# Optimization experiments

Measured on AMD Instinct MI355X. Metric: run time of the kernel, lower is better.

The kernel has to match this reference:

```python
import jax, jax.numpy as jnp
from jax import lax
import numpy as np
import math

V, D, N, L, KC, KL, B, S = 32000, 1024, 64, 4, 4, 4, 2, 1024
SCALE = 1.0 / math.sqrt(2 * L)   # base_layer.residual_scale
GAMMA = 0.01                     # lindblad_gamma
COND_TH = 100.0                  # condition_threshold
PHASE = np.complex64(np.exp(1j * 0.1))  # quaternionic escape rotation


def setup_inputs() -> dict:
    key = jax.random.key(0)
    ks = jax.random.split(key, 16)
    g = lambda k, shp, s=0.02: jax.random.normal(k, shp, jnp.float32) * s
    return {
        'token_ids': jax.random.randint(ks[0], (B, S), 0, V, dtype=jnp.int32),
        'emb_r': g(ks[1], (V, D)),
        'emb_i': g(ks[2], (V, D)),
        'W_in': g(ks[3], (L, D, 2 * D)),
        'conv_k': g(ks[4], (L, D, KC), 0.2),
        'A_log': jax.random.normal(ks[5], (L, D, N), jnp.float32) * 0.5,
        'dt_scale': g(ks[6], (L, D), 1.0),
        'dt_bias': jnp.full((L, D), -2.0, jnp.float32),
        'W_B': g(ks[7], (L, N, D)),
        'W_C': g(ks[8], (L, N, D)),
        'D_skip': g(ks[9], (L, D), 0.1),
        'W_out': g(ks[10], (L, D, D)),
        'L_ops': g(ks[11], (L, KL, D), 0.1),
        'norm_w': jnp.ones((D,), jnp.float32),
    }


def _dwconv(x, k):
    # causal depthwise conv; x [B,S,D] real, k [D,KC]
    xt = jnp.transpose(x, (0, 2, 1))  # [B,D,S]
    pad = k.shape[-1] - 1
    y = lax.conv_general_dilated(xt, k[:, None, :], (1,), [(pad, 0)],
                                 feature_group_count=k.shape[0])
    return jnp.transpose(y, (0, 2, 1))


def _csilu(x):
    # complex 'silu': x * sigmoid(|x|)
    return x * jax.nn.sigmoid(jnp.abs(x))


def _layer(x, Wi, ck, Alog, dts, dtb, WB, WC, Dk, Wo, Lops):
    residual = x
    xz = jnp.einsum('bsd,de->bse', x, Wi)          # complex [B,S,2D]
    x1, z = xz[..., :D], xz[..., D:]
    x1 = _dwconv(x1.real, ck) + 1j * _dwconv(x1.imag, ck)
    x1 = _csilu(x1)
    dt = jax.nn.softplus(x1.real * dts + dtb)      # [B,S,D] real
    A = -jnp.exp(Alog)                             # [D,N] real, stable
    Bc = jnp.einsum('bsd,nd->bsn', x1, WB)         # complex [B,S,N]
    Cc = jnp.einsum('bsd,nd->bsn', x1, WC)

    def step(h, inp):
        dt_t, x_t, B_t, C_t = inp                  # [B,D],[B,D],[B,N],[B,N]
        decay = jnp.exp(dt_t[..., None] * A)       # [B,D,N] real
        h = decay * h + (dt_t * x_t)[..., None] * B_t[:, None, :]
        y = jnp.einsum('bdn,bn->bd', h, C_t)
        return h, y

    h0 = jnp.zeros((x.shape[0], D, N), jnp.complex64)
    xs = (jnp.transpose(dt, (1, 0, 2)), jnp.transpose(x1, (1, 0, 2)),
          jnp.transpose(Bc, (1, 0, 2)), jnp.transpose(Cc, (1, 0, 2)))
    _, ys = lax.scan(step, h0, xs)                 # [S,B,D]
    y = jnp.transpose(ys, (1, 0, 2)) + Dk * x1
    y = y * _csilu(z)
    branch = jnp.einsum('bsd,de->bse', y, Wo)      # branch_out = (out-res)/scale

    # Lindblad dissipation: psi -> psi - gamma * sum_k L_k (L_k^H psi)
    proj = jnp.einsum('bsd,kd->bsk', branch, Lops)
    branch = branch - GAMMA * jnp.einsum('bsk,kd->bsd', proj, Lops)

    # H_eff = mean_s |psi_s><psi_s|; quaternionic escape uses its conditioning.
    # Only the diagonal is needed for the (diag-approx) condition number.
    diag = jnp.mean(jnp.abs(branch) ** 2, axis=1)  # [B,D]
    cond = jnp.max(diag, -1) / (jnp.min(diag, -1) + 1e-8)
    phase = jnp.where(cond > COND_TH, PHASE, jnp.complex64(1.0))  # [B]
    branch = branch * phase[:, None, None]

    # hybrid automata: _H_prev is None on first forward -> no jump (faithful)
    return residual + SCALE * branch


def reference(token_ids, emb_r, emb_i, W_in, conv_k, A_log, dt_scale, dt_bias,
              W_B, W_C, D_skip, W_out, L_ops, norm_w):
    psi = emb_r[token_ids] + 1j * emb_i[token_ids]   # [B,S,D] complex64
    for l in range(L):
        psi = _layer(psi, W_in[l], conv_k[l], A_log[l], dt_scale[l],
                     dt_bias[l], W_B[l], W_C[l], D_skip[l], W_out[l], L_ops[l])
    # ComplexRMSNorm
    rms = jnp.sqrt(jnp.mean(jnp.abs(psi) ** 2, -1, keepdims=True) + 1e-8)
    psi = psi / rms * norm_w
    # Born collapse sampler with weight tied to real embedding
    amp_r = jnp.einsum('bsd,vd->bsv', psi.real, emb_r)
    amp_i = jnp.einsum('bsd,vd->bsv', psi.imag, emb_r)
    logits = jnp.log(amp_r ** 2 + amp_i ** 2 + 1e-8)  # [B,S,V] real
    return logits
```

## Files before the change

kernel.cpp:

```cpp
#include <hip/hip_runtime.h>
#include <math.h>

#define BB 2
#define SS 1024
#define DD 1024
#define NN 64
#define LLAYERS 4
#define KCC 4
#define KLL 4
#define VV 32000
#define MM (BB*SS)
#define M2 (2*MM)
#define PS ((size_t)MM*DD)
#define CH 4
#define LC (SS/CH)
#define BDW (BB*DD)

#define SCALE_F 0.35355339059327373f
#define GAMMA_F 0.01f
#define PHASE_COS 0.99500416527802576f
#define PHASE_SIN 0.09983341664682815f

typedef _Float16 f16x8 __attribute__((ext_vector_type(8)));
typedef _Float16 f16x4 __attribute__((ext_vector_type(4)));
typedef float f32x4 __attribute__((ext_vector_type(4)));

__device__ __forceinline__ float softplus_f(float x) {
    return fmaxf(x, 0.f) + log1pf(expf(-fabsf(x)));
}

__device__ __forceinline__ void async16(void* lds_dst, const void* g_src) {
    __builtin_amdgcn_global_load_lds(
        (const __attribute__((address_space(1))) unsigned int*)g_src,
        (__attribute__((address_space(3))) unsigned int*)lds_dst,
        16, 0, 0);
}

__device__ __forceinline__ float rsum64_dpp(float v) {
    int x;
    x = __float_as_int(v);
    v += __int_as_float(__builtin_amdgcn_update_dpp(0, x, 0x111, 0xf, 0xf, true));
    x = __float_as_int(v);
    v += __int_as_float(__builtin_amdgcn_update_dpp(0, x, 0x112, 0xf, 0xf, true));
    x = __float_as_int(v);
    v += __int_as_float(__builtin_amdgcn_update_dpp(0, x, 0x114, 0xf, 0xf, true));
    x = __float_as_int(v);
    v += __int_as_float(__builtin_amdgcn_update_dpp(0, x, 0x118, 0xf, 0xf, true));
    x = __float_as_int(v);
    v += __int_as_float(__builtin_amdgcn_update_dpp(0, x, 0x142, 0xa, 0xf, true));
    x = __float_as_int(v);
    v += __int_as_float(__builtin_amdgcn_update_dpp(0, x, 0x143, 0xc, 0xf, true));
    return v;
}

__global__ __launch_bounds__(256) void k_split_w(const float* __restrict__ W,
        _Float16* __restrict__ Wh, _Float16* __restrict__ Wl, int Ksz, int Nsz) {
    __shared__ float t[32][33];
    int k0 = blockIdx.x * 32, n0 = blockIdx.y * 32;
    size_t base = (size_t)blockIdx.z * Ksz * Nsz;
    int r = threadIdx.x >> 3, c4 = (threadIdx.x & 7) * 4;
    float4 v = *(const float4*)(W + base + (size_t)(k0 + r) * Nsz + n0 + c4);
    t[r][c4 + 0] = v.x; t[r][c4 + 1] = v.y; t[r][c4 + 2] = v.z; t[r][c4 + 3] = v.w;
    __syncthreads();
    f16x4 hi, lo;
    #pragma unroll
    for (int j = 0; j < 4; ++j) {
        float x = t[c4 + j][r];
        _Float16 h = (_Float16)x;
        hi[j] = h; lo[j] = (_Float16)(x - (float)h);
    }
    size_t o = base + (size_t)(n0 + r) * Ksz + k0 + c4;
    *(f16x4*)(Wh + o) = hi;
    *(f16x4*)(Wl + o) = lo;
}

__global__ __launch_bounds__(256) void k_embed(const int* __restrict__ tok,
        const float* __restrict__ er, const float* __restrict__ ei,
        float* __restrict__ Pr, float* __restrict__ Pi,
        _Float16* __restrict__ Ph, _Float16* __restrict__ Pl) {
    int i = blockIdx.x * 256 + threadIdx.x;
    int d4 = (i & (DD/4 - 1)) * 4;
    int m  = i >> 8;
    int t = tok[m];
    float4 r  = *(const float4*)(er + (size_t)t * DD + d4);
    float4 im = *(const float4*)(ei + (size_t)t * DD + d4);
    size_t o = (size_t)m * DD + d4;
    *(float4*)(Pr + o) = r;
    *(float4*)(Pi + o) = im;
    float vr[4] = {r.x, r.y, r.z, r.w}, vi[4] = {im.x, im.y, im.z, im.w};
    f16x4 rh, rl, ih, il;
    #pragma unroll
    for (int j = 0; j < 4; ++j) {
        _Float16 h = (_Float16)vr[j]; rh[j] = h; rl[j] = (_Float16)(vr[j] - (float)h);
        _Float16 g = (_Float16)vi[j]; ih[j] = g; il[j] = (_Float16)(vi[j] - (float)g);
    }
    *(f16x4*)(Ph + o) = rh;      *(f16x4*)(Pl + o) = rl;
    *(f16x4*)(Ph + PS + o) = ih; *(f16x4*)(Pl + PS + o) = il;
}

__global__ __launch_bounds__(256, 2) void k_gemm_f16(
        const _Float16* __restrict__ Ah, const _Float16* __restrict__ Al,
        const _Float16* __restrict__ Bh, const _Float16* __restrict__ Bl,
        float* __restrict__ C, int Nsz) {
    __shared__ __align__(16) unsigned char lds[32768];
    const int lane = threadIdx.x & 63;
    const int wid  = threadIdx.x >> 6;
    const int wm = (wid >> 1) * 64;
    const int wv = (wid & 1) * 64;
    const int n0 = blockIdx.x * 128;
    const int m0 = blockIdx.y * 128;
    const int fr = lane & 15, fq = lane >> 4;

    f32x4 acc[4][4] = {};

    for (int k0 = 0; k0 < 1024; k0 += 32) {
        #pragma unroll
        for (int j = 0; j < 8; ++j) {
            int cid = wid * 8 + j;
            int sel = cid >> 3, c = cid & 7;
            const _Float16* bp = (sel == 0) ? Ah : (sel == 1) ? Al : (sel == 2) ? Bh : Bl;
            int rbase = ((sel < 2) ? m0 : n0) + c * 16 + fr;
            async16(lds + cid * 1024, bp + (size_t)rbase * 1024 + k0 + fq * 8);
        }
        __syncthreads();

        f16x8 ah[4], al[4];
        #pragma unroll
        for (int ms = 0; ms < 4; ++ms) {
            int off = ((wm >> 4) + ms) * 1024 + lane * 16;
            ah[ms] = *(const f16x8*)(lds + off);
            al[ms] = *(const f16x8*)(lds + 8192 + off);
        }
        #pragma unroll
        for (int vs = 0; vs < 4; ++vs) {
            int boff = ((wv >> 4) + vs) * 1024 + lane * 16;
            f16x8 bh = *(const f16x8*)(lds + 16384 + boff);
            f16x8 bl = *(const f16x8*)(lds + 24576 + boff);
            #pragma unroll
            for (int ms = 0; ms < 4; ++ms) {
                acc[ms][vs] = __builtin_amdgcn_mfma_f32_16x16x32_f16(ah[ms], bh, acc[ms][vs], 0, 0, 0);
                acc[ms][vs] = __builtin_amdgcn_mfma_f32_16x16x32_f16(ah[ms], bl, acc[ms][vs], 0, 0, 0);
                acc[ms][vs] = __builtin_amdgcn_mfma_f32_16x16x32_f16(al[ms], bh, acc[ms][vs], 0, 0, 0);
            }
        }
        __syncthreads();
    }

    #pragma unroll
    for (int ms = 0; ms < 4; ++ms) {
        #pragma unroll
        for (int vs = 0; vs < 4; ++vs) {
            #pragma unroll
            for (int r = 0; r < 4; ++r) {
                int row = m0 + wm + ms * 16 + fq * 4 + r;
                int col = n0 + wv + vs * 16 + fr;
                C[(size_t)row * Nsz + col] = acc[ms][vs][r];
            }
        }
    }
}

__global__ __launch_bounds__(256, 2) void k_gemm_n64(
        const _Float16* __restrict__ Ah, const _Float16* __restrict__ Al,
        const _Float16* __restrict__ Bh, const _Float16* __restrict__ Bl,
        float* __restrict__ C, int Nsz) {
    __shared__ __align__(16) unsigned char lds[24576];
    const int lane = threadIdx.x & 63;
    const int wid  = threadIdx.x >> 6;
    const int wm = (wid >> 1) * 64;
    const int wv = (wid & 1) * 32;
    const int n0 = blockIdx.x * 64;
    const int m0 = blockIdx.y * 128;
    const int fr = lane & 15, fq = lane >> 4;

    f32x4 acc[4][2] = {};

    for (int k0 = 0; k0 < 1024; k0 += 32) {
        #pragma unroll
        for (int j = 0; j < 6; ++j) {
            int cid = j * 4 + wid;
            const _Float16* bp;
            int rbase, ldsoff;
            if (cid < 16) {
                bp = (cid >> 3) ? Al : Ah;
                rbase = m0 + (cid & 7) * 16 + fr;
                ldsoff = cid * 1024;
            } else {
                int r = cid - 16;
                bp = (r >> 2) ? Bl : Bh;
                rbase = n0 + (r & 3) * 16 + fr;
                ldsoff = 16384 + r * 1024;
            }
            async16(lds + ldsoff, bp + (size_t)rbase * 1024 + k0 + fq * 8);
        }
        __syncthreads();

        f16x8 ah[4], al[4];
        #pragma unroll
        for (int ms = 0; ms < 4; ++ms) {
            int off = ((wm >> 4) + ms) * 1024 + lane * 16;
            ah[ms] = *(const f16x8*)(lds + off);
            al[ms] = *(const f16x8*)(lds + 8192 + off);
        }
        #pragma unroll
        for (int vs = 0; vs < 2; ++vs) {
            int boff = ((wv >> 4) + vs) * 1024 + lane * 16;
            f16x8 bh = *(const f16x8*)(lds + 16384 + boff);
            f16x8 bl = *(const f16x8*)(lds + 20480 + boff);
            #pragma unroll
            for (int ms = 0; ms < 4; ++ms) {
                acc[ms][vs] = __builtin_amdgcn_mfma_f32_16x16x32_f16(ah[ms], bh, acc[ms][vs], 0, 0, 0);
                acc[ms][vs] = __builtin_amdgcn_mfma_f32_16x16x32_f16(ah[ms], bl, acc[ms][vs], 0, 0, 0);
                acc[ms][vs] = __builtin_amdgcn_mfma_f32_16x16x32_f16(al[ms], bh, acc[ms][vs], 0, 0, 0);
            }
        }
        __syncthreads();
    }

    #pragma unroll
    for (int ms = 0; ms < 4; ++ms) {
        #pragma unroll
        for (int vs = 0; vs < 2; ++vs) {
            #pragma unroll
            for (int r = 0; r < 4; ++r) {
                int row = m0 + wm + ms * 16 + fq * 4 + r;
                int col = n0 + wv + vs * 16 + fr;
                C[(size_t)row * Nsz + col] = acc[ms][vs][r];
            }
        }
    }
}

__global__ __launch_bounds__(256) void k_conv(const float* __restrict__ XZ,
        const float* __restrict__ ck, const float* __restrict__ dts,
        const float* __restrict__ dtb,
        float* __restrict__ Xr, float* __restrict__ Xi, float* __restrict__ DT,
        float* __restrict__ ZUr, float* __restrict__ ZUi) {
    int i4 = blockIdx.x * 256 + threadIdx.x;
    int dq = (i4 & (DD / 4 - 1)) * 4;
    int m  = i4 >> 8;
    int b = m >> 10, s = m & (SS - 1);
    size_t i = (size_t)m * DD + dq;
    float kw[4][4];
    #pragma unroll
    for (int c = 0; c < 4; ++c)
        *(float4*)kw[c] = *(const float4*)(ck + (size_t)(dq + c) * KCC);
    float cr[4] = {0.f, 0.f, 0.f, 0.f}, ci[4] = {0.f, 0.f, 0.f, 0.f};
    #pragma unroll
    for (int j = 0; j < KCC; ++j) {
        int sj = s - (KCC - 1) + j;
        if (sj >= 0) {
            size_t mm = ((size_t)(b << 10) + sj) * 2048 + dq;
            float4 xr4 = *(const float4*)(XZ + mm);
            float4 xi4 = *(const float4*)(XZ + (size_t)MM * 2048 + mm);
            float xr_[4] = {xr4.x, xr4.y, xr4.z, xr4.w};
            float xi_[4] = {xi4.x, xi4.y, xi4.z, xi4.w};
            #pragma unroll
            for (int c = 0; c < 4; ++c) {
                cr[c] = fmaf(xr_[c], kw[c][j], cr[c]);
                ci[c] = fmaf(xi_[c], kw[c][j], ci[c]);
            }
        }
    }
    float4 dts4 = *(const float4*)(dts + dq);
    float4 dtb4 = *(const float4*)(dtb + dq);
    float dts_[4] = {dts4.x, dts4.y, dts4.z, dts4.w};
    float dtb_[4] = {dtb4.x, dtb4.y, dtb4.z, dtb4.w};
    float xro[4], xio[4], dto[4];
    #pragma unroll
    for (int c = 0; c < 4; ++c) {
        float mag = sqrtf(cr[c] * cr[c] + ci[c] * ci[c]);
        float sg = 1.f / (1.f + expf(-mag));
        xro[c] = cr[c] * sg; xio[c] = ci[c] * sg;
        dto[c] = softplus_f(fmaf(xro[c], dts_[c], dtb_[c]));
    }
    *(float4*)(Xr + i) = make_float4(xro[0], xro[1], xro[2], xro[3]);
    *(float4*)(Xi + i) = make_float4(xio[0], xio[1], xio[2], xio[3]);
    *(float4*)(DT + i) = make_float4(dto[0], dto[1], dto[2], dto[3]);
    float4 zr4 = *(const float4*)(XZ + (size_t)m * 2048 + DD + dq);
    float4 zi4 = *(const float4*)(XZ + (size_t)(MM + m) * 2048 + DD + dq);
    float zr_[4] = {zr4.x, zr4.y, zr4.z, zr4.w};
    float zi_[4] = {zi4.x, zi4.y, zi4.z, zi4.w};
    float zur[4], zui[4];
    #pragma unroll
    for (int c = 0; c < 4; ++c) {
        float mz = sqrtf(zr_[c] * zr_[c] + zi_[c] * zi_[c]);
        float sz = 1.f / (1.f + expf(-mz));
        zur[c] = zr_[c] * sz; zui[c] = zi_[c] * sz;
    }
    *(float4*)(ZUr + i) = make_float4(zur[0], zur[1], zur[2], zur[3]);
    *(float4*)(ZUi + i) = make_float4(zui[0], zui[1], zui[2], zui[3]);
}

__global__ __launch_bounds__(256) void k_bc(const float* __restrict__ X,
        const float* __restrict__ WBp, const float* __restrict__ WCp,
        float* __restrict__ BC2) {
    __shared__ float xs[4][DD];
    __shared__ float red[4 * 256];
    int r0 = blockIdx.x * 4;
    for (int f = threadIdx.x; f < 4 * (DD / 4); f += 256) {
        int r = f / (DD / 4), c = (f % (DD / 4)) * 4;
        *(float4*)(&xs[r][c]) = *(const float4*)(X + (size_t)(r0 + r) * DD + c);
    }
    __syncthreads();
    int out = threadIdx.x & 127;
    int half = threadIdx.x >> 7;
    const float* Wrow = (out < 64) ? (WBp + (size_t)out * DD) : (WCp + (size_t)(out - 64) * DD);
    float acc[4] = {0.f, 0.f, 0.f, 0.f};
    for (int k = half * 512; k < half * 512 + 512; k += 4) {
        float4 w = *(const float4*)(Wrow + k);
        #pragma unroll
        for (int r = 0; r < 4; ++r) {
            float4 x4 = *(float4*)(&xs[r][k]);
            acc[r] = fmaf(x4.x, w.x, fmaf(x4.y, w.y, fmaf(x4.z, w.z, fmaf(x4.w, w.w, acc[r]))));
        }
    }
    #pragma unroll
    for (int r = 0; r < 4; ++r) red[r * 256 + threadIdx.x] = acc[r];
    __syncthreads();
    if (threadIdx.x < 128) {
        int isIm = (r0 >= MM) ? 1 : 0;
        int n = out & 63;
        int comp = ((out >> 6) << 1) | isIm;
        #pragma unroll
        for (int r = 0; r < 4; ++r) {
            float v = red[r * 256 + threadIdx.x] + red[r * 256 + threadIdx.x + 128];
            int m = (r0 + r) & (MM - 1);
            BC2[((size_t)m * 64 + n) * 4 + comp] = v;
        }
    }
}

__global__ __launch_bounds__(256, 8) void k_scan1(const float* __restrict__ X,
        const float* __restrict__ DT, const float4* __restrict__ BC2,
        const float* __restrict__ Alog, float* __restrict__ Y2T,
        float2* __restrict__ HB, float* __restrict__ SDT) {
    int w = (blockIdx.x << 2) + (threadIdx.x >> 6);
    int lane = threadIdx.x & 63;
    int c = w & (CH - 1);
    int bd = w >> 2;
    int b = bd >> 10, d = bd & (DD - 1);
    float Av = -__expf(Alog[(size_t)d * NN + lane]);
    float hr = 0.f, hi = 0.f, sdt = 0.f;
    int s0 = c * LC, s1 = s0 + LC;
    size_t mBase = (size_t)(b << 10);
    size_t md = (mBase + s0) * DD + d;
    float dt_c = DT[md], xr_c = X[md], xi_c = X[PS + md];
    float4 bc_c = BC2[(mBase + s0) * 64 + lane];
    size_t ys = (size_t)bd * SS + s0;
    for (int s = s0; s < s1; ++s) {
        int sn = (s + 1 < s1) ? (s + 1) : s;
        size_t mdn = (mBase + sn) * DD + d;
        float dt_n = DT[mdn], xr_n = X[mdn], xi_n = X[PS + mdn];
        float4 bc_n = BC2[(mBase + sn) * 64 + lane];
        float g = __expf(dt_c * Av);
        float dxr = dt_c * xr_c, dxi = dt_c * xi_c;
        hr = fmaf(g, hr, fmaf(dxr, bc_c.x, -dxi * bc_c.y));
        hi = fmaf(g, hi, fmaf(dxr, bc_c.y,  dxi * bc_c.x));
        sdt += dt_c;
        float yr = rsum64_dpp(hr * bc_c.z - hi * bc_c.w);
        float yi = rsum64_dpp(hr * bc_c.w + hi * bc_c.z);
        if (lane == 63) {
            Y2T[ys]      = yr;
            Y2T[PS + ys] = yi;
        }
        ++ys;
        dt_c = dt_n; xr_c = xr_n; xi_c = xi_n; bc_c = bc_n;
    }
    HB[((size_t)c * BDW + bd) * NN + lane] = make_float2(hr, hi);
    if (lane == 0) SDT[c * BDW + bd] = sdt;
}

__global__ __launch_bounds__(256, 8) void k_scan3(const float* __restrict__ DT,
        const float* __restrict__ BC2, const float* __restrict__ Alog,
        const float2* __restrict__ HB, const float* __restrict__ SDT,
        float* __restrict__ Y2T) {
    int w = (blockIdx.x << 2) + (threadIdx.x >> 6);
    int lane = threadIdx.x & 63;
    int cm1 = w >> 11;
    int bd = w & (BDW - 1);
    int b = bd >> 10, d = bd & (DD - 1);
    float Av = -__expf(Alog[(size_t)d * NN + lane]);
    float2 h0 = HB[(size_t)bd * NN + lane];
    float hr = h0.x, hi = h0.y;
    if (cm1 >= 1) {
        float2 h1 = HB[((size_t)1 * BDW + bd) * NN + lane];
        float P1 = __expf(Av * SDT[1 * BDW + bd]);
        hr = fmaf(P1, hr, h1.x); hi = fmaf(P1, hi, h1.y);
        if (cm1 >= 2) {
            float2 h2 = HB[((size_t)2 * BDW + bd) * NN + lane];
            float P2 = __expf(Av * SDT[2 * BDW + bd]);
            hr = fmaf(P2, hr, h2.x); hi = fmaf(P2, hi, h2.y);
        }
    }
    int s0 = (cm1 + 1) * LC, s1 = s0 + LC;
    size_t mBase = (size_t)(b << 10);
    size_t md = (mBase + s0) * DD + d;
    float dt_c = DT[md];
    float2 cc_c = *(const float2*)(BC2 + ((mBase + s0) * 64 + lane) * 4 + 2);
    size_t ys = (size_t)bd * SS + s0;
    for (int s = s0; s < s1; ++s) {
        int sn = (s + 1 < s1) ? (s + 1) : s;
        size_t mdn = (mBase + sn) * DD + d;
        float dt_n = DT[mdn];
        float2 cc_n = *(const float2*)(BC2 + ((mBase + sn) * 64 + lane) * 4 + 2);
        float g = __expf(dt_c * Av);
        hr *= g; hi *= g;
        float yr = rsum64_dpp(hr * cc_c.x - hi * cc_c.y);
        float yi = rsum64_dpp(hr * cc_c.y + hi * cc_c.x);
        if (lane == 63) {
            Y2T[ys]      += yr;
            Y2T[PS + ys] += yi;
        }
        ++ys;
        dt_c = dt_n; cc_c = cc_n;
    }
}

__global__ __launch_bounds__(256) void k_ymod(const float* __restrict__ Y2T,
        const float* __restrict__ X, const float* __restrict__ ZUr,
        const float* __restrict__ ZUi, const float* __restrict__ Dk,
        _Float16* __restrict__ YOh, _Float16* __restrict__ YOl) {
    __shared__ float tr[64][65];
    __shared__ float ti[64][65];
    int d0 = blockIdx.x * 64, m0 = blockIdx.y * 64;
    int b = m0 >> 10, s0 = m0 & (SS - 1);
    int t = threadIdx.x;
    int rr = t >> 2, c0 = (t & 3) * 4;
    size_t ybase = (size_t)(b * DD + d0 + rr) * SS + s0;
    #pragma unroll
    for (int j = 0; j < 4; ++j) {
        float4 vr = *(const float4*)(Y2T + ybase + c0 + j * 16);
        float4 vi = *(const float4*)(Y2T + PS + ybase + c0 + j * 16);
        int sl = c0 + j * 16;
        tr[sl + 0][rr] = vr.x; tr[sl + 1][rr] = vr.y; tr[sl + 2][rr] = vr.z; tr[sl + 3][rr] = vr.w;
        ti[sl + 0][rr] = vi.x; ti[sl + 1][rr] = vi.y; ti[sl + 2][rr] = vi.z; ti[sl + 3][rr] = vi.w;
    }
    __syncthreads();
    int td = t & 63, tq = t >> 6;
    float dk = Dk[d0 + td];
    #pragma unroll
    for (int k = 0; k < 16; ++k) {
        int tm = tq * 16 + k;
        size_t i = (size_t)(m0 + tm) * DD + d0 + td;
        float yr = tr[tm][td];
        float yi = ti[tm][td];
        yr = fmaf(dk, X[i], yr);
        yi = fmaf(dk, X[PS + i], yi);
        float zr = ZUr[i], zi = ZUi[i];
        float or_ = yr * zr - yi * zi;
        float oi_ = yr * zi + yi * zr;
        _Float16 h0 = (_Float16)or_, h1 = (_Float16)oi_;
        YOh[i] = h0;      YOl[i] = (_Float16)(or_ - (float)h0);
        YOh[PS + i] = h1; YOl[PS + i] = (_Float16)(oi_ - (float)h1);
    }
}

__global__ __launch_bounds__(256) void k_projcorr(float* __restrict__ BR,
        const float* __restrict__ Lop) {
    int row = (blockIdx.x << 2) + (threadIdx.x >> 6);
    int lane = threadIdx.x & 63;
    float* br = BR + (size_t)row * DD;
    float4 v[4], lw[4][4];
    float acc[4] = {0.f, 0.f, 0.f, 0.f};
    #pragma unroll
    for (int j = 0; j < 4; ++j) {
        int col = lane * 4 + j * 256;
        v[j] = *(const float4*)(br + col);
        #pragma unroll
        for (int k = 0; k < 4; ++k) {
            lw[j][k] = *(const float4*)(Lop + (size_t)k * DD + col);
            acc[k] += v[j].x * lw[j][k].x + v[j].y * lw[j][k].y
                    + v[j].z * lw[j][k].z + v[j].w * lw[j][k].w;
        }
    }
    #pragma unroll
    for (int off = 1; off <= 32; off <<= 1) {
        #pragma unroll
        for (int k = 0; k < 4; ++k) acc[k] += __shfl_xor(acc[k], off, 64);
    }
    #pragma unroll
    for (int j = 0; j < 4; ++j) {
        int col = lane * 4 + j * 256;
        float4 o;
        o.x = v[j].x - GAMMA_F * (acc[0]*lw[j][0].x + acc[1]*lw[j][1].x + acc[2]*lw[j][2].x + acc[3]*lw[j][3].x);
        o.y = v[j].y - GAMMA_F * (acc[0]*lw[j][0].y + acc[1]*lw[j][1].y + acc[2]*lw[j][2].y + acc[3]*lw[j][3].y);
        o.z = v[j].z - GAMMA_F * (acc[0]*lw[j][0].z + acc[1]*lw[j][1].z + acc[2]*lw[j][2].z + acc[3]*lw[j][3].z);
        o.w = v[j].w - GAMMA_F * (acc[0]*lw[j][0].w + acc[1]*lw[j][1].w + acc[2]*lw[j][2].w + acc[3]*lw[j][3].w);
        *(float4*)(br + col) = o;
    }
}

__global__ __launch_bounds__(256) void k_diag(const float* __restrict__ BR,
        float* __restrict__ DG) {
    __shared__ float red[4][64];
    int b = blockIdx.y, d0 = blockIdx.x * 64;
    int sg = threadIdx.x >> 6, ld = threadIdx.x & 63;
    float acc = 0.f;
    for (int s = sg; s < SS; s += 4) {
        size_t m = (size_t)(b * SS + s) * DD + d0 + ld;
        float r = BR[m], ii = BR[PS + m];
        acc = fmaf(r, r, fmaf(ii, ii, acc));
    }
    red[sg][ld] = acc;
    __syncthreads();
    if (threadIdx.x < 64) {
        float v = red[0][threadIdx.x] + red[1][threadIdx.x] + red[2][threadIdx.x] + red[3][threadIdx.x];
        DG[b * DD + d0 + threadIdx.x] = v * (1.f / SS);
    }
}

__global__ __launch_bounds__(256) void k_phase(const float* __restrict__ DG,
        float* __restrict__ PH) {
    __shared__ float mx[256], mn[256];
    int b = blockIdx.x;
    float vmax = -1e30f, vmin = 1e30f;
    for (int d = threadIdx.x; d < DD; d += 256) {
        float v = DG[b * DD + d];
        vmax = fmaxf(vmax, v); vmin = fminf(vmin, v);
    }
    mx[threadIdx.x] = vmax; mn[threadIdx.x] = vmin;
    __syncthreads();
    for (int st = 128; st >= 1; st >>= 1) {
        if (threadIdx.x < st) {
            mx[threadIdx.x] = fmaxf(mx[threadIdx.x], mx[threadIdx.x + st]);
            mn[threadIdx.x] = fminf(mn[threadIdx.x], mn[threadIdx.x + st]);
        }
        __syncthreads();
    }
    if (threadIdx.x == 0) {
        float cond = mx[0] / (mn[0] + 1e-8f);
        bool ap = cond > 100.0f;
        PH[b * 2 + 0] = ap ? PHASE_COS : 1.f;
        PH[b * 2 + 1] = ap ? PHASE_SIN : 0.f;
    }
}

__global__ __launch_bounds__(256) void k_resid(float* __restrict__ Pr,
        float* __restrict__ Pi, const float* __restrict__ BR,
        const float* __restrict__ PH,
        _Float16* __restrict__ Ph, _Float16* __restrict__ Pl) {
    size_t i = ((size_t)blockIdx.x * 256 + threadIdx.x) * 4;
    int b = (int)(i >> 20);
    float pr = PH[b * 2], pih = PH[b * 2 + 1];
    float4 brr4 = *(const float4*)(BR + i);
    float4 bri4 = *(const float4*)(BR + PS + i);
    float4 pr4  = *(const float4*)(Pr + i);
    float4 pi4  = *(const float4*)(Pi + i);
    float brr[4] = {brr4.x, brr4.y, brr4.z, brr4.w};
    float bri[4] = {bri4.x, bri4.y, bri4.z, bri4.w};
    float pro[4] = {pr4.x, pr4.y, pr4.z, pr4.w};
    float pio[4] = {pi4.x, pi4.y, pi4.z, pi4.w};
    f16x4 rh, rl, ih, il;
    float nr[4], ni[4];
    #pragma unroll
    for (int c = 0; c < 4; ++c) {
        nr[c] = fmaf(SCALE_F, brr[c] * pr - bri[c] * pih, pro[c]);
        ni[c] = fmaf(SCALE_F, brr[c] * pih + bri[c] * pr, pio[c]);
        _Float16 h0 = (_Float16)nr[c]; rh[c] = h0; rl[c] = (_Float16)(nr[c] - (float)h0);
        _Float16 h1 = (_Float16)ni[c]; ih[c] = h1; il[c] = (_Float16)(ni[c] - (float)h1);
    }
    *(float4*)(Pr + i) = make_float4(nr[0], nr[1], nr[2], nr[3]);
    *(float4*)(Pi + i) = make_float4(ni[0], ni[1], ni[2], ni[3]);
    *(f16x4*)(Ph + i) = rh;      *(f16x4*)(Pl + i) = rl;
    *(f16x4*)(Ph + PS + i) = ih; *(f16x4*)(Pl + PS + i) = il;
}

__global__ __launch_bounds__(256) void k_rms(const float* __restrict__ Pr,
        const float* __restrict__ Pi, const float* __restrict__ nw,
        _Float16* __restrict__ Sp) {
    __shared__ float red[256];
    int m = blockIdx.x;
    int d = threadIdx.x * 4;
    float4 r  = *(const float4*)(Pr + (size_t)m * DD + d);
    float4 ii = *(const float4*)(Pi + (size_t)m * DD + d);
    float acc = r.x*r.x + r.y*r.y + r.z*r.z + r.w*r.w
              + ii.x*ii.x + ii.y*ii.y + ii.z*ii.z + ii.w*ii.w;
    red[threadIdx.x] = acc;
    __syncthreads();
    for (int st = 128; st >= 1; st >>= 1) {
        if (threadIdx.x < st) red[threadIdx.x] += red[threadIdx.x + st];
        __syncthreads();
    }
    float inv = 1.f / sqrtf(red[0] * (1.f / DD) + 1e-8f);
    float4 w = *(const float4*)(nw + d);
    float qr[4] = {r.x*inv*w.x, r.y*inv*w.y, r.z*inv*w.z, r.w*inv*w.w};
    float qi[4] = {ii.x*inv*w.x, ii.y*inv*w.y, ii.z*inv*w.z, ii.w*inv*w.w};
    f16x4 rh, rl, ih, il;
    #pragma unroll
    for (int j = 0; j < 4; ++j) {
        _Float16 h = (_Float16)qr[j]; rh[j] = h; rl[j] = (_Float16)(qr[j] - (float)h);
        _Float16 g = (_Float16)qi[j]; ih[j] = g; il[j] = (_Float16)(qi[j] - (float)g);
    }
    size_t o = (size_t)m * DD + d;
    *(f16x4*)(Sp + o)          = rh;
    *(f16x4*)(Sp + PS + o)     = rl;
    *(f16x4*)(Sp + 2 * PS + o) = ih;
    *(f16x4*)(Sp + 3 * PS + o) = il;
}

__global__ __launch_bounds__(256) void k_split_e(const float* __restrict__ E,
        _Float16* __restrict__ Eh, _Float16* __restrict__ El) {
    size_t i = (size_t)(blockIdx.x * 256 + threadIdx.x) * 8;
    float4 a = *(const float4*)(E + i);
    float4 b = *(const float4*)(E + i + 4);
    float v[8] = {a.x, a.y, a.z, a.w, b.x, b.y, b.z, b.w};
    f16x8 hi, lo;
    #pragma unroll
    for (int j = 0; j < 8; ++j) {
        _Float16 h = (_Float16)v[j];
        hi[j] = h; lo[j] = (_Float16)(v[j] - (float)h);
    }
    *(f16x8*)(Eh + i) = hi;
    *(f16x8*)(El + i) = lo;
}

__global__ __launch_bounds__(256, 2) void k_logits_mfma(
        const _Float16* __restrict__ Sp,
        const _Float16* __restrict__ Eh, const _Float16* __restrict__ El,
        float* __restrict__ out) {
    __shared__ __align__(16) unsigned char lds[49152];
    const int lane = threadIdx.x & 63;
    const int wid  = threadIdx.x >> 6;
    const int wm = (wid >> 1) * 64;
    const int wv = (wid & 1) * 64;
    const int fr = lane & 15, fq = lane >> 4;
    int x = blockIdx.x & 7;
    int j = blockIdx.x >> 3;
    const int m0 = ((x << 1) | (j & 1)) << 7;
    const int v0 = (j >> 1) << 7;

    f32x4 accR[4][4] = {};
    f32x4 accI[4][4] = {};

    for (int k0 = 0; k0 < DD; k0 += 32) {
        #pragma unroll
        for (int jj = 0; jj < 12; ++jj) {
            int cid = jj * 4 + wid;
            const _Float16* src;
            int ldsoff;
            if (cid < 32) {
                int p = cid >> 3, c = cid & 7;
                src = Sp + (size_t)p * PS + (size_t)(m0 + c * 16 + fr) * DD + k0 + fq * 8;
                ldsoff = p * 8192 + c * 1024;
            } else {
                int r = cid - 32;
                int q = r >> 3, c = r & 7;
                const _Float16* Ep = q ? El : Eh;
                src = Ep + (size_t)(v0 + c * 16 + fr) * DD + k0 + fq * 8;
                ldsoff = 32768 + q * 8192 + c * 1024;
            }
            async16(lds + ldsoff, src);
        }
        __syncthreads();

        f16x8 aRh[4], aRl[4], aIh[4], aIl[4];
        #pragma unroll
        for (int ms = 0; ms < 4; ++ms) {
            int off = ((wm >> 4) + ms) * 1024 + lane * 16;
            aRh[ms] = *(const f16x8*)(lds + off);
            aRl[ms] = *(const f16x8*)(lds + 8192 + off);
            aIh[ms] = *(const f16x8*)(lds + 16384 + off);
            aIl[ms] = *(const f16x8*)(lds + 24576 + off);
        }
        #pragma unroll
        for (int vs = 0; vs < 4; ++vs) {
            int boff = ((wv >> 4) + vs) * 1024 + lane * 16;
            f16x8 bh = *(const f16x8*)(lds + 32768 + boff);
            f16x8 bl = *(const f16x8*)(lds + 40960 + boff);
            #pragma unroll
            for (int ms = 0; ms < 4; ++ms) {
                accR[ms][vs] = __builtin_amdgcn_mfma_f32_16x16x32_f16(aRh[ms], bh, accR[ms][vs], 0, 0, 0);
                accR[ms][vs] = __builtin_amdgcn_mfma_f32_16x16x32_f16(aRh[ms], bl, accR[ms][vs], 0, 0, 0);
                accR[ms][vs] = __builtin_amdgcn_mfma_f32_16x16x32_f16(aRl[ms], bh, accR[ms][vs], 0, 0, 0);
                accI[ms][vs] = __builtin_amdgcn_mfma_f32_16x16x32_f16(aIh[ms], bh, accI[ms][vs], 0, 0, 0);
                accI[ms][vs] = __builtin_amdgcn_mfma_f32_16x16x32_f16(aIh[ms], bl, accI[ms][vs], 0, 0, 0);
                accI[ms][vs] = __builtin_amdgcn_mfma_f32_16x16x32_f16(aIl[ms], bh, accI[ms][vs], 0, 0, 0);
            }
        }
        __syncthreads();
    }

    #pragma unroll
    for (int ms = 0; ms < 4; ++ms) {
        #pragma unroll
        for (int vs = 0; vs < 4; ++vs) {
            #pragma unroll
            for (int r = 0; r < 4; ++r) {
                int row = m0 + wm + ms * 16 + fq * 4 + r;
                int col = v0 + wv + vs * 16 + fr;
                float ar = accR[ms][vs][r], ai = accI[ms][vs][r];
                __builtin_nontemporal_store(logf(fmaf(ar, ar, fmaf(ai, ai, 1e-8f))),
                                            out + (size_t)row * VV + col);
            }
        }
    }
}

extern "C" void kernel_launch(void* const* d_in, const int* in_sizes, int n_in,
                              void* d_out, int out_size, void* d_ws, size_t ws_size,
                              hipStream_t stream) {
    const int*   tok  = (const int*)d_in[0];
    const float* er   = (const float*)d_in[1];
    const float* ei   = (const float*)d_in[2];
    const float* Win  = (const float*)d_in[3];
    const float* ck   = (const float*)d_in[4];
    const float* Alog = (const float*)d_in[5];
    const float* dts  = (const float*)d_in[6];
    const float* dtb  = (const float*)d_in[7];
    const float* WB   = (const float*)d_in[8];
    const float* WC   = (const float*)d_in[9];
    const float* Dk   = (const float*)d_in[10];
    const float* Wo   = (const float*)d_in[11];
    const float* Lop  = (const float*)d_in[12];
    const float* nw   = (const float*)d_in[13];
    float* out = (float*)d_out;

    float* W0   = (float*)d_ws;
    float* P    = W0;
    float* XZ   = W0 + 2 * PS;
    float* X    = W0 + 6 * PS;
    float* DTp  = W0 + 8 * PS;
    float* ZU   = W0 + 9 * PS;
    float* Y2T  = W0 + 11 * PS;
    _Float16* YOh = (_Float16*)(W0 + 19 * PS);
    _Float16* YOl = (_Float16*)(W0 + 20 * PS);
    _Float16* Ph  = (_Float16*)(W0 + 21 * PS);
    _Float16* Pl  = (_Float16*)(W0 + 22 * PS);
    float* BR   = XZ;
    float* BC2  = W0 + 23 * PS;
    float* DIAG = BC2 + (size_t)MM * 64 * 4;
    float* PH   = DIAG + BB * DD;
    float2* HB  = (float2*)(PH + 16);
    float* SDT  = (float*)(HB + (size_t)CH * BDW * NN);
    _Float16* Winh = (_Float16*)(W0 + 25 * PS);
    _Float16* Winl = (_Float16*)(W0 + 27 * PS);
    _Float16* Woh  = (_Float16*)(W0 + 29 * PS);
    _Float16* Wol  = (_Float16*)(W0 + 30 * PS);
    _Float16* Sp  = (_Float16*)(W0 + 2 * PS);
    _Float16* Ehp = (_Float16*)(W0 + 4 * PS);
    _Float16* Elp = (_Float16*)(W0 + 13 * PS);

    k_split_w<<<dim3(32, 64, 4), 256, 0, stream>>>(Win, Winh, Winl, 1024, 2048);
    k_split_w<<<dim3(32, 32, 4), 256, 0, stream>>>(Wo, Woh, Wol, 1024, 1024);

    k_embed<<<(int)(PS / 4 / 256), 256, 0, stream>>>(tok, er, ei, P, P + PS, Ph, Pl);

    for (int l = 0; l < LLAYERS; ++l) {
        const float* Lopl = Lop + (size_t)l * KLL * DD;
        const float* Alogl = Alog + (size_t)l * DD * NN;
        const _Float16* Wih = Winh + (size_t)l * 2048 * 1024;
        const _Float16* Wil = Winl + (size_t)l * 2048 * 1024;
        const _Float16* Wohl = Woh + (size_t)l * 1024 * 1024;
        const _Float16* Woll = Wol + (size_t)l * 1024 * 1024;

        k_gemm_f16<<<dim3(2048 / 128, M2 / 128), 256, 0, stream>>>(Ph, Pl, Wih, Wil, XZ, 2048);
        k_conv<<<(int)(MM * (size_t)DD / 4 / 256), 256, 0, stream>>>(XZ, ck + (size_t)l * DD * KCC,
                dts + l * DD, dtb + l * DD, X, X + PS, DTp, ZU, ZU + PS);
        k_bc<<<M2 / 4, 256, 0, stream>>>(X, WB + (size_t)l * NN * DD, WC + (size_t)l * NN * DD, BC2);
        k_scan1<<<(BDW * CH) / 4, 256, 0, stream>>>(X, DTp, (const float4*)BC2, Alogl, Y2T, HB, SDT);
        k_scan3<<<(BDW * 3) / 4, 256, 0, stream>>>(DTp, BC2, Alogl, HB, SDT, Y2T);
        k_ymod<<<dim3(DD / 64, MM / 64), 256, 0, stream>>>(Y2T, X, ZU, ZU + PS, Dk + l * DD, YOh, YOl);
        k_gemm_n64<<<dim3(1024 / 64, M2 / 128), 256, 0, stream>>>(YOh, YOl, Wohl, Woll, BR, 1024);
        k_projcorr<<<M2 / 4, 256, 0, stream>>>(BR, Lopl);
        k_diag<<<dim3(DD / 64, BB), 256, 0, stream>>>(BR, DIAG);
        k_phase<<<BB, 256, 0, stream>>>(DIAG, PH);
        k_resid<<<(int)(PS / 4 / 256), 256, 0, stream>>>(P, P + PS, BR, PH, Ph, Pl);
    }

    k_rms<<<MM, 256, 0, stream>>>(P, P + PS, nw, Sp);
    k_split_e<<<(int)((size_t)VV * DD / 8 / 256), 256, 0, stream>>>(er, Ehp, Elp);
    k_logits_mfma<<<4000, 256, 0, stream>>>(Sp, Ehp, Elp, out);
}
```

Baseline: 3.594 ms.

## Process four channels per wavefront in chunked scan to reuse B/C loads

The chunked selective-scan kernels now give each wavefront four adjacent D channels instead of one. Each per-timestep B/C vector load is shared across the four channels, and dt/x are read as float4. This cuts redundant global traffic on BC2 and the per-step load latency per channel, at the cost of 4x fewer wavefronts and more registers, which may hurt latency hiding. The logits store also drops its nontemporal hint and becomes a plain store, and a parameter is renamed to avoid a clash with the new macro.

```diff
diff --git a/kernel.cpp b/kernel.cpp
--- a/kernel.cpp
+++ b/kernel.cpp
@@ -15,6 +15,7 @@
 #define CH 4
 #define LC (SS/CH)
 #define BDW (BB*DD)
+#define DG 4
 
 #define SCALE_F 0.35355339059327373f
 #define GAMMA_F 0.01f
@@ -331,86 +332,115 @@
     }
 }
 
-__global__ __launch_bounds__(256, 8) void k_scan1(const float* __restrict__ X,
+__global__ __launch_bounds__(256) void k_scan1(const float* __restrict__ X,
         const float* __restrict__ DT, const float4* __restrict__ BC2,
         const float* __restrict__ Alog, float* __restrict__ Y2T,
         float2* __restrict__ HB, float* __restrict__ SDT) {
     int w = (blockIdx.x << 2) + (threadIdx.x >> 6);
     int lane = threadIdx.x & 63;
     int c = w & (CH - 1);
-    int bd = w >> 2;
-    int b = bd >> 10, d = bd & (DD - 1);
-    float Av = -__expf(Alog[(size_t)d * NN + lane]);
-    float hr = 0.f, hi = 0.f, sdt = 0.f;
+    int grp = w >> 2;
+    int b = grp >> 8;
+    int d0 = (grp & 255) << 2;
+    float Av[DG], hr[DG], hi[DG], sdt[DG];
+    #pragma unroll
+    for (int j = 0; j < DG; ++j) {
+        Av[j] = -__expf(Alog[(size_t)(d0 + j) * NN + lane]);
+        hr[j] = 0.f; hi[j] = 0.f; sdt[j] = 0.f;
+    }
     int s0 = c * LC, s1 = s0 + LC;
     size_t mBase = (size_t)(b << 10);
-    size_t md = (mBase + s0) * DD + d;
-    float dt_c = DT[md], xr_c = X[md], xi_c = X[PS + md];
+    size_t md = (mBase + s0) * DD + d0;
+    float4 dt_c = *(const float4*)(DT + md);
+    float4 xr_c = *(const float4*)(X + md);
+    float4 xi_c = *(const float4*)(X + PS + md);
     float4 bc_c = BC2[(mBase + s0) * 64 + lane];
-    size_t ys = (size_t)bd * SS + s0;
+    size_t ys = ((size_t)(b << 10) + d0) * SS + s0;
     for (int s = s0; s < s1; ++s) {
         int sn = (s + 1 < s1) ? (s + 1) : s;
-        size_t mdn = (mBase + sn) * DD + d;
-        float dt_n = DT[mdn], xr_n = X[mdn], xi_n = X[PS + mdn];
+        size_t mdn = (mBase + sn) * DD + d0;
+        float4 dt_n = *(const float4*)(DT + mdn);
+        float4 xr_n = *(const float4*)(X + mdn);
+        float4 xi_n = *(const float4*)(X + PS + mdn);
         float4 bc_n = BC2[(mBase + sn) * 64 + lane];
-        float g = __expf(dt_c * Av);
-        float dxr = dt_c * xr_c, dxi = dt_c * xi_c;
-        hr = fmaf(g, hr, fmaf(dxr, bc_c.x, -dxi * bc_c.y));
-        hi = fmaf(g, hi, fmaf(dxr, bc_c.y,  dxi * bc_c.x));
-        sdt += dt_c;
-        float yr = rsum64_dpp(hr * bc_c.z - hi * bc_c.w);
-        float yi = rsum64_dpp(hr * bc_c.w + hi * bc_c.z);
-        if (lane == 63) {
-            Y2T[ys]      = yr;
-            Y2T[PS + ys] = yi;
+        float dtv[4] = {dt_c.x, dt_c.y, dt_c.z, dt_c.w};
+        float xrv[4] = {xr_c.x, xr_c.y, xr_c.z, xr_c.w};
+        float xiv[4] = {xi_c.x, xi_c.y, xi_c.z, xi_c.w};
+        #pragma unroll
+        for (int j = 0; j < DG; ++j) {
+            float g = __expf(dtv[j] * Av[j]);
+            float dxr = dtv[j] * xrv[j], dxi = dtv[j] * xiv[j];
+            hr[j] = fmaf(g, hr[j], fmaf(dxr, bc_c.x, -dxi * bc_c.y));
+            hi[j] = fmaf(g, hi[j], fmaf(dxr, bc_c.y,  dxi * bc_c.x));
+            sdt[j] += dtv[j];
+            float yr = rsum64_dpp(hr[j] * bc_c.z - hi[j] * bc_c.w);
+            float yi = rsum64_dpp(hr[j] * bc_c.w + hi[j] * bc_c.z);
+            if (lane == 63) {
+                Y2T[ys + (size_t)j * SS]      = yr;
+                Y2T[PS + ys + (size_t)j * SS] = yi;
+            }
         }
         ++ys;
         dt_c = dt_n; xr_c = xr_n; xi_c = xi_n; bc_c = bc_n;
     }
-    HB[((size_t)c * BDW + bd) * NN + lane] = make_float2(hr, hi);
-    if (lane == 0) SDT[c * BDW + bd] = sdt;
-}
-
-__global__ __launch_bounds__(256, 8) void k_scan3(const float* __restrict__ DT,
+    #pragma unroll
+    for (int j = 0; j < DG; ++j) {
+        int bd = (b << 10) + d0 + j;
+        HB[((size_t)c * BDW + bd) * NN + lane] = make_float2(hr[j], hi[j]);
+        if (lane == 0) SDT[c * BDW + bd] = sdt[j];
+    }
+}
+
+__global__ __launch_bounds__(256) void k_scan3(const float* __restrict__ DT,
         const float* __restrict__ BC2, const float* __restrict__ Alog,
         const float2* __restrict__ HB, const float* __restrict__ SDT,
         float* __restrict__ Y2T) {
     int w = (blockIdx.x << 2) + (threadIdx.x >> 6);
     int lane = threadIdx.x & 63;
-    int cm1 = w >> 11;
-    int bd = w & (BDW - 1);
-    int b = bd >> 10, d = bd & (DD - 1);
-    float Av = -__expf(Alog[(size_t)d * NN + lane]);
-    float2 h0 = HB[(size_t)bd * NN + lane];
-    float hr = h0.x, hi = h0.y;
-    if (cm1 >= 1) {
-        float2 h1 = HB[((size_t)1 * BDW + bd) * NN + lane];
-        float P1 = __expf(Av * SDT[1 * BDW + bd]);
-        hr = fmaf(P1, hr, h1.x); hi = fmaf(P1, hi, h1.y);
-        if (cm1 >= 2) {
-            float2 h2 = HB[((size_t)2 * BDW + bd) * NN + lane];
-            float P2 = __expf(Av * SDT[2 * BDW + bd]);
-            hr = fmaf(P2, hr, h2.x); hi = fmaf(P2, hi, h2.y);
+    int cm1 = w >> 9;
+    int grp = w & 511;
+    int b = grp >> 8;
+    int d0 = (grp & 255) << 2;
+    float Av[DG], hr[DG], hi[DG];
+    #pragma unroll
+    for (int j = 0; j < DG; ++j) {
+        int bd = (b << 10) + d0 + j;
+        Av[j] = -__expf(Alog[(size_t)(d0 + j) * NN + lane]);
+        float2 h0 = HB[(size_t)bd * NN + lane];
+        hr[j] = h0.x; hi[j] = h0.y;
+        if (cm1 >= 1) {
+            float2 h1 = HB[((size_t)1 * BDW + bd) * NN + lane];
+            float P1 = __expf(Av[j] * SDT[1 * BDW + bd]);
+            hr[j] = fmaf(P1, hr[j], h1.x); hi[j] = fmaf(P1, hi[j], h1.y);
+            if (cm1 >= 2) {
+                float2 h2 = HB[((size_t)2 * BDW + bd) * NN + lane];
+                float P2 = __expf(Av[j] * SDT[2 * BDW + bd]);
+                hr[j] = fmaf(P2, hr[j], h2.x); hi[j] = fmaf(P2, hi[j], h2.y);
+            }
         }
     }
     int s0 = (cm1 + 1) * LC, s1 = s0 + LC;
     size_t mBase = (size_t)(b << 10);
-    size_t md = (mBase + s0) * DD + d;
-    float dt_c = DT[md];
+    size_t md = (mBase + s0) * DD + d0;
+    float4 dt_c = *(const float4*)(DT + md);
     float2 cc_c = *(const float2*)(BC2 + ((mBase + s0) * 64 + lane) * 4 + 2);
-    size_t ys = (size_t)bd * SS + s0;
+    size_t ys = ((size_t)(b << 10) + d0) * SS + s0;
     for (int s = s0; s < s1; ++s) {
         int sn = (s + 1 < s1) ? (s + 1) : s;
-        size_t mdn = (mBase + sn) * DD + d;
-        float dt_n = DT[mdn];
+        size_t mdn = (mBase + sn) * DD + d0;
+        float4 dt_n = *(const float4*)(DT + mdn);
         float2 cc_n = *(const float2*)(BC2 + ((mBase + sn) * 64 + lane) * 4 + 2);
-        float g = __expf(dt_c * Av);
-        hr *= g; hi *= g;
-        float yr = rsum64_dpp(hr * cc_c.x - hi * cc_c.y);
-        float yi = rsum64_dpp(hr * cc_c.y + hi * cc_c.x);
-        if (lane == 63) {
-            Y2T[ys]      += yr;
-            Y2T[PS + ys] += yi;
+        float dtv[4] = {dt_c.x, dt_c.y, dt_c.z, dt_c.w};
+        #pragma unroll
+        for (int j = 0; j < DG; ++j) {
+            float g = __expf(dtv[j] * Av[j]);
+            hr[j] *= g; hi[j] *= g;
+            float yr = rsum64_dpp(hr[j] * cc_c.x - hi[j] * cc_c.y);
+            float yi = rsum64_dpp(hr[j] * cc_c.y + hi[j] * cc_c.x);
+            if (lane == 63) {
+                Y2T[ys + (size_t)j * SS]      += yr;
+                Y2T[PS + ys + (size_t)j * SS] += yi;
+            }
         }
         ++ys;
         dt_c = dt_n; cc_c = cc_n;
@@ -492,7 +522,7 @@
 }
 
 __global__ __launch_bounds__(256) void k_diag(const float* __restrict__ BR,
-        float* __restrict__ DG) {
+        float* __restrict__ DG_) {
     __shared__ float red[4][64];
     int b = blockIdx.y, d0 = blockIdx.x * 64;
     int sg = threadIdx.x >> 6, ld = threadIdx.x & 63;
@@ -506,17 +536,17 @@
     __syncthreads();
     if (threadIdx.x < 64) {
         float v = red[0][threadIdx.x] + red[1][threadIdx.x] + red[2][threadIdx.x] + red[3][threadIdx.x];
-        DG[b * DD + d0 + threadIdx.x] = v * (1.f / SS);
-    }
-}
-
-__global__ __launch_bounds__(256) void k_phase(const float* __restrict__ DG,
+        DG_[b * DD + d0 + threadIdx.x] = v * (1.f / SS);
+    }
+}
+
+__global__ __launch_bounds__(256) void k_phase(const float* __restrict__ DG_,
         float* __restrict__ PH) {
     __shared__ float mx[256], mn[256];
     int b = blockIdx.x;
     float vmax = -1e30f, vmin = 1e30f;
     for (int d = threadIdx.x; d < DD; d += 256) {
-        float v = DG[b * DD + d];
+        float v = DG_[b * DD + d];
         vmax = fmaxf(vmax, v); vmin = fminf(vmin, v);
     }
     mx[threadIdx.x] = vmax; mn[threadIdx.x] = vmin;
@@ -690,8 +720,7 @@
                 int row = m0 + wm + ms * 16 + fq * 4 + r;
                 int col = v0 + wv + vs * 16 + fr;
                 float ar = accR[ms][vs][r], ai = accI[ms][vs][r];
-                __builtin_nontemporal_store(logf(fmaf(ar, ar, fmaf(ai, ai, 1e-8f))),
-                                            out + (size_t)row * VV + col);
+                out[(size_t)row * VV + col] = logf(fmaf(ar, ar, fmaf(ai, ai, 1e-8f)));
             }
         }
     }
@@ -758,8 +787,8 @@
         k_conv<<<(int)(MM * (size_t)DD / 4 / 256), 256, 0, stream>>>(XZ, ck + (size_t)l * DD * KCC,
                 dts + l * DD, dtb + l * DD, X, X + PS, DTp, ZU, ZU + PS);
         k_bc<<<M2 / 4, 256, 0, stream>>>(X, WB + (size_t)l * NN * DD, WC + (size_t)l * NN * DD, BC2);
-        k_scan1<<<(BDW * CH) / 4, 256, 0, stream>>>(X, DTp, (const float4*)BC2, Alogl, Y2T, HB, SDT);
-        k_scan3<<<(BDW * 3) / 4, 256, 0, stream>>>(DTp, BC2, Alogl, HB, SDT, Y2T);
+        k_scan1<<<(BDW / DG) * CH / 4, 256, 0, stream>>>(X, DTp, (const float4*)BC2, Alogl, Y2T, HB, SDT);
+        k_scan3<<<(BDW / DG) * 3 / 4, 256, 0, stream>>>(DTp, BC2, Alogl, HB, SDT, Y2T);
         k_ymod<<<dim3(DD / 64, MM / 64), 256, 0, stream>>>(Y2T, X, ZU, ZU + PS, Dk + l * DD, YOh, YOl);
         k_gemm_n64<<<dim3(1024 / 64, M2 / 128), 256, 0, stream>>>(YOh, YOl, Wohl, Woll, BR, 1024);
         k_projcorr<<<M2 / 4, 256, 0, stream>>>(BR, Lopl);
```

New measurement: 4.246 ms. 1.18x slower.
